# Kernel optimization log

Measured on AMD Instinct MI355X. Metric: run time of the kernel, lower is better.

The kernel has to match this reference:

```python
import jax, jax.numpy as jnp
import numpy as np

B, C, H, W = 32, 1536, 24, 24
HID, D, K = 512, 128, 64  # hidden, cluster_dim, num_clusters


def setup_inputs() -> dict:
    key = jax.random.key(0)
    ks = jax.random.split(key, 6)
    def rn(k, shape, scale):
        return jax.random.normal(k, shape, dtype=jnp.float32) * scale
    return {
        "x": rn(ks[0], (B, C, H, W), 1.0),
        # cluster_features: Conv2d(C,512,1) -> ReLU -> Conv2d(512,D,1)
        "w1c": rn(ks[1], (HID, C), 0.02), "b1c": jnp.zeros((HID,), jnp.float32),
        "w2c": rn(ks[2], (D, HID), 0.02), "b2c": jnp.zeros((D,), jnp.float32),
        # score: Conv2d(C,512,1) -> ReLU -> Conv2d(512,K,1)
        "w1s": rn(ks[3], (HID, C), 0.02), "b1s": jnp.zeros((HID,), jnp.float32),
        "w2s": rn(ks[4], (K, HID), 0.02), "b2s": jnp.zeros((K,), jnp.float32),
        "temperature": jnp.array(1.0, jnp.float32),
    }


def _sinkhorn_log(S, num_iters=3):
    # log-domain OT solver with uniform marginals log(1/n), reg=1 (M/reg == M)
    b, m, n = S.shape
    norm = -jnp.log(jnp.asarray(n, S.dtype))
    log_a = jnp.full((b, m), norm, S.dtype)
    log_b = jnp.full((b, n), norm, S.dtype)
    u = jnp.zeros((b, m), S.dtype)
    v = jnp.zeros((b, n), S.dtype)
    for _ in range(num_iters):
        u = log_a - jax.nn.logsumexp(S + v[:, None, :], axis=2)
        v = log_b - jax.nn.logsumexp(S + u[:, :, None], axis=1)
    # get_matching_probs subtracts norm at the end
    return S + u[:, :, None] + v[:, None, :] - norm


def reference(x, w1c, b1c, w2c, b2c, w1s, b1s, w2s, b2s, temperature):
    b, c, h, w = x.shape
    xf = x.reshape(b, c, h * w)  # (B, C, N); 1x1 conv == channel GEMM
    # cluster features f: (B, D, N)
    hc = jax.nn.relu(jnp.einsum('oc,bcn->bon', w1c, xf) + b1c[None, :, None])
    f = jnp.einsum('oc,bcn->bon', w2c, hc) + b2c[None, :, None]
    # assignment scores p: (B, K, N)
    hs = jax.nn.relu(jnp.einsum('oc,bcn->bon', w1s, xf) + b1s[None, :, None])
    s = jnp.einsum('oc,bcn->bon', w2s, hs) + b2s[None, :, None]
    log_p = _sinkhorn_log(s, num_iters=3)
    p = jnp.exp(log_p / temperature) + jnp.exp(log_p)  # (B, K, N)
    # (f.unsqueeze(2) * p.unsqueeze(1)).sum(-1) == batched matmul
    agg = jnp.einsum('bcn,bkn->bck', f, p)  # (B, D, K)
    flat = agg.reshape(b, -1)
    nrm = jnp.maximum(jnp.linalg.norm(flat, axis=-1, keepdims=True), 1e-12)
    return flat / nrm
```

## Files before the change

kernel.cpp:

```cpp
#include <hip/hip_runtime.h>

typedef unsigned short ushort_t;
typedef float f32x4 __attribute__((ext_vector_type(4)));
typedef short short8 __attribute__((ext_vector_type(8)));

#define B_   32
#define C_   1536
#define N_   576
#define HID_ 512
#define D_   128
#define K_   64

__device__ __forceinline__ float bf2f(ushort_t u) {
    union { unsigned u; float f; } c; c.u = ((unsigned)u) << 16; return c.f;
}
__device__ __forceinline__ ushort_t f2bf(float x) {
    unsigned u = __float_as_uint(x);
    return (ushort_t)((u + 0x7FFFu + ((u >> 16) & 1u)) >> 16);
}

typedef const __attribute__((address_space(1))) char gas_char;
typedef __attribute__((address_space(3))) char las_char;
__device__ __forceinline__ void cp16(const void* g, void* l) {
    __builtin_amdgcn_global_load_lds((gas_char*)(size_t)g,
                                     (las_char*)(unsigned)(size_t)l, 16, 0, 0);
}
__device__ __forceinline__ void bar() {
    asm volatile("" ::: "memory");
    __builtin_amdgcn_s_barrier();
    asm volatile("" ::: "memory");
}

#define OB1_  1572864
#define OW2C_ 1573888
#define OB2C_ 1639424
#define OW2S_ 1639552
#define OB2S_ 1672320
#define WTOT_ 1672384
#define TRB2_ 3456
#define CVB4_ (((WTOT_ / 4) + 255) / 256)

__global__ __launch_bounds__(256) void prep_kernel(
    const void* __restrict__ x,
    const void* __restrict__ w1c, const void* __restrict__ b1c,
    const void* __restrict__ w2c, const void* __restrict__ b2c,
    const void* __restrict__ w1s, const void* __restrict__ b1s,
    const void* __restrict__ w2s, const void* __restrict__ b2s,
    const unsigned* __restrict__ temp,
    ushort_t* __restrict__ xt, ushort_t* __restrict__ o, float* __restrict__ Tp)
{
    __shared__ ushort_t t[128][65];
    unsigned d = temp[0];
    int flag = (d == 0x3F800000u) ? 1 : 0;
    int tid = threadIdx.x;
    int idx = blockIdx.x;
    if (idx == 0 && tid == 0)
        *Tp = flag ? __uint_as_float(d) : bf2f((ushort_t)(d & 0xFFFFu));

    if (idx < TRB2_) {
        int b = idx / 108, rem = idx % 108;
        int c0 = (rem % 12) * 128, n0 = (rem / 12) * 64;
        ushort_t* xtb = xt + (size_t)b * N_ * C_;
        int r = tid >> 4, n4 = (tid & 15) * 4;
        if (flag) {
            const float* xb = (const float*)x + (size_t)b * C_ * N_;
#pragma unroll
            for (int i = 0; i < 8; ++i) {
                int cc = r + i * 16;
                float4 v = *(const float4*)&xb[(size_t)(c0 + cc) * N_ + n0 + n4];
                t[cc][n4 + 0] = f2bf(v.x);
                t[cc][n4 + 1] = f2bf(v.y);
                t[cc][n4 + 2] = f2bf(v.z);
                t[cc][n4 + 3] = f2bf(v.w);
            }
        } else {
            const ushort_t* xb = (const ushort_t*)x + (size_t)b * C_ * N_;
#pragma unroll
            for (int i = 0; i < 8; ++i) {
                int cc = r + i * 16;
                *(uint2*)&t[cc][n4] =
                    *(const uint2*)&xb[(size_t)(c0 + cc) * N_ + n0 + n4];
            }
        }
        __syncthreads();
        int c8 = (tid & 15) * 8;
#pragma unroll
        for (int i = 0; i < 4; ++i) {
            int nn = r + i * 16;
            ushort_t vv[8];
#pragma unroll
            for (int j = 0; j < 8; ++j) vv[j] = t[c8 + j][nn];
            uint4 o4;
            o4.x = (unsigned)vv[0] | ((unsigned)vv[1] << 16);
            o4.y = (unsigned)vv[2] | ((unsigned)vv[3] << 16);
            o4.z = (unsigned)vv[4] | ((unsigned)vv[5] << 16);
            o4.w = (unsigned)vv[6] | ((unsigned)vv[7] << 16);
            *(uint4*)&xtb[(size_t)(n0 + nn) * C_ + c0 + c8] = o4;
        }
    } else {
        int i4 = ((idx - TRB2_) * 256 + tid) * 4;
        if (i4 >= WTOT_) return;
        const void* p; int off;
        if      (i4 < 786432)  { p = w1c; off = i4; }
        else if (i4 < OB1_)    { p = w1s; off = i4 - 786432; }
        else if (i4 < 1573376) { p = b1c; off = i4 - OB1_; }
        else if (i4 < OW2C_)   { p = b1s; off = i4 - 1573376; }
        else if (i4 < OB2C_)   { p = w2c; off = i4 - OW2C_; }
        else if (i4 < OW2S_)   { p = b2c; off = i4 - OB2C_; }
        else if (i4 < OB2S_)   { p = w2s; off = i4 - OW2S_; }
        else                   { p = b2s; off = i4 - OB2S_; }
        if (flag) {
            float4 v = *(const float4*)((const float*)p + off);
            uint2 r;
            r.x = (unsigned)f2bf(v.x) | ((unsigned)f2bf(v.y) << 16);
            r.y = (unsigned)f2bf(v.z) | ((unsigned)f2bf(v.w) << 16);
            *(uint2*)&o[i4] = r;
        } else {
            *(uint2*)&o[i4] = *(const uint2*)((const ushort_t*)p + off);
        }
    }
}

__global__ __launch_bounds__(256) void gemm1_kernel(
    const ushort_t* __restrict__ Xt, const ushort_t* __restrict__ W1,
    const ushort_t* __restrict__ bias, ushort_t* __restrict__ h)
{
    __shared__ ushort_t Atile[2][128 * 64];
    __shared__ ushort_t Btile[2][128 * 64];
    int idx = blockIdx.x;
    int l = (idx & 7) * 144 + (idx >> 3);
    int mt = l >> 3, t = l & 7;
    int row0 = mt * 128, col0 = t * 128;

    int tid = threadIdx.x, w = tid >> 6, lane = tid & 63;
    int wr = w >> 1, wc = w & 1;
    int r16 = lane & 15, q = lane >> 4, kh = q * 8;

    int srow = tid >> 3;
    int cx = ((tid & 7) ^ (srow & 7)) * 8;
    const ushort_t* ag[4];
    const ushort_t* bg[4];
#pragma unroll
    for (int s = 0; s < 4; ++s) {
        ag[s] = Xt + (size_t)(row0 + s * 32 + srow) * C_ + cx;
        bg[s] = W1 + (size_t)(col0 + s * 32 + srow) * C_ + cx;
    }

    f32x4 acc[4][4];
#pragma unroll
    for (int i = 0; i < 4; ++i)
#pragma unroll
        for (int j = 0; j < 4; ++j) acc[i][j] = f32x4{0.f, 0.f, 0.f, 0.f};

    int rowa = wr * 64 + r16;
    int rowb = wc * 64 + r16;
    int xr = (r16 & 7) * 8;

    auto stage = [&](int buf, int koff) {
#pragma unroll
        for (int s = 0; s < 4; ++s) {
            cp16(ag[s] + koff, &Atile[buf][tid * 8 + s * 2048]);
            cp16(bg[s] + koff, &Btile[buf][tid * 8 + s * 2048]);
        }
    };
    auto compute = [&](int cb) {
#pragma unroll
        for (int ks = 0; ks < 2; ++ks) {
            int ke = (ks * 32 + kh) ^ xr;
            short8 af[4], bf[4];
#pragma unroll
            for (int i = 0; i < 4; ++i)
                af[i] = *(const short8*)&Atile[cb][(rowa + i * 16) * 64 + ke];
#pragma unroll
            for (int j = 0; j < 4; ++j)
                bf[j] = *(const short8*)&Btile[cb][(rowb + j * 16) * 64 + ke];
#pragma unroll
            for (int i = 0; i < 4; ++i)
#pragma unroll
                for (int j = 0; j < 4; ++j)
                    acc[i][j] = __builtin_amdgcn_mfma_f32_16x16x32_bf16(
                        af[i], bf[j], acc[i][j], 0, 0, 0);
        }
    };

    stage(0, 0);
#pragma unroll
    for (int kt = 0; kt < 24; ++kt) {
        int buf = kt & 1;
        if (kt < 23) {
            stage(buf ^ 1, (kt + 1) * 64);
            asm volatile("s_waitcnt vmcnt(8)" ::: "memory");
        } else {
            asm volatile("s_waitcnt vmcnt(0)" ::: "memory");
        }
        bar();
        compute(buf);
        bar();
    }

#pragma unroll
    for (int j = 0; j < 4; ++j) {
        int col = col0 + wc * 64 + j * 16 + r16;
        float cb = bf2f(bias[col]);
#pragma unroll
        for (int i = 0; i < 4; ++i) {
            int rowo = row0 + wr * 64 + i * 16 + q * 4;
#pragma unroll
            for (int r = 0; r < 4; ++r) {
                float v = fmaxf(acc[i][j][r] + cb, 0.f);
                h[(size_t)(rowo + r) * 1024 + col] = f2bf(v);
            }
        }
    }
}

__global__ __launch_bounds__(256) void gemm2_kernel(
    const ushort_t* __restrict__ Wb, const ushort_t* __restrict__ h,
    ushort_t* __restrict__ fbuf, float* __restrict__ sbuf)
{
    __shared__ ushort_t Atile[2][128 * 32];
    __shared__ ushort_t Btile[2][128 * 32];
    int nt = blockIdx.x, b = blockIdx.y, z = blockIdx.z;
    int col0 = nt * 128;
    int Mclamp = z ? K_ : D_;
    const ushort_t* Aw   = Wb + (z ? OW2S_ : OW2C_);
    const ushort_t* bias = Wb + (z ? OB2S_ : OB2C_);
    const ushort_t* hb = h + (size_t)b * N_ * 1024 + (z ? 512 : 0);

    int tid = threadIdx.x, w = tid >> 6, lane = tid & 63;
    int wr = w >> 1, wc = w & 1;
    int r16 = lane & 15, q = lane >> 4, kh = q * 8;

    int srow = tid >> 2;
    int swz = ((tid & 3) ^ (srow & 3)) * 8;
    int ar0 = min(srow, Mclamp - 1);
    int ar1 = min(64 + srow, Mclamp - 1);
    const ushort_t* ag0 = Aw + (size_t)ar0 * HID_ + swz;
    const ushort_t* ag1 = Aw + (size_t)ar1 * HID_ + swz;
    int br0 = min(col0 + srow, N_ - 1);
    int br1 = min(col0 + 64 + srow, N_ - 1);
    const ushort_t* bg0 = hb + (size_t)br0 * 1024 + swz;
    const ushort_t* bg1 = hb + (size_t)br1 * 1024 + swz;

    f32x4 acc[4][4];
#pragma unroll
    for (int i = 0; i < 4; ++i)
#pragma unroll
        for (int j = 0; j < 4; ++j) acc[i][j] = f32x4{0.f, 0.f, 0.f, 0.f};

    int xr = (r16 & 3) * 8;

    auto stage = [&](int buf, int koff) {
        cp16(ag0 + koff, &Atile[buf][tid * 8]);
        cp16(ag1 + koff, &Atile[buf][2048 + tid * 8]);
        cp16(bg0 + koff, &Btile[buf][tid * 8]);
        cp16(bg1 + koff, &Btile[buf][2048 + tid * 8]);
    };
    auto compute = [&](int cb) {
        int ke = kh ^ xr;
        short8 af[4], bf[4];
#pragma unroll
        for (int i = 0; i < 4; ++i)
            af[i] = *(const short8*)&Atile[cb][(wr * 64 + i * 16 + r16) * 32 + ke];
#pragma unroll
        for (int j = 0; j < 4; ++j)
            bf[j] = *(const short8*)&Btile[cb][(wc * 64 + j * 16 + r16) * 32 + ke];
#pragma unroll
        for (int i = 0; i < 4; ++i)
#pragma unroll
            for (int j = 0; j < 4; ++j)
                acc[i][j] = __builtin_amdgcn_mfma_f32_16x16x32_bf16(
                    af[i], bf[j], acc[i][j], 0, 0, 0);
    };

    stage(0, 0);
#pragma unroll
    for (int kt = 0; kt < 16; ++kt) {
        int buf = kt & 1;
        if (kt < 15) {
            stage(buf ^ 1, (kt + 1) * 32);
            asm volatile("s_waitcnt vmcnt(4)" ::: "memory");
        } else {
            asm volatile("s_waitcnt vmcnt(0)" ::: "memory");
        }
        bar();
        compute(buf);
        bar();
    }

#pragma unroll
    for (int j = 0; j < 4; ++j) {
        int col = col0 + wc * 64 + j * 16 + r16;
#pragma unroll
        for (int i = 0; i < 4; ++i) {
            int rowb = wr * 64 + i * 16 + q * 4;
#pragma unroll
            for (int r = 0; r < 4; ++r) {
                int rr = rowb + r;
                if (rr < Mclamp && col < N_) {
                    float v = acc[i][j][r] + bf2f(bias[rr]);
                    if (z == 0)
                        fbuf[(size_t)b * D_ * N_ + (size_t)rr * N_ + col] = f2bf(v);
                    else
                        sbuf[(size_t)b * K_ * N_ + (size_t)rr * N_ + col] = v;
                }
            }
        }
    }
}

__global__ __launch_bounds__(512) void tail_kernel(
    const ushort_t* __restrict__ f_all, const float* __restrict__ s_all,
    const float* __restrict__ Tp, const unsigned* __restrict__ temp,
    void* __restrict__ out)
{
    __shared__ float Sl[K_ * 577];
    __shared__ float su[K_];
    __shared__ float sv[N_];
    __shared__ float red[8];
    ushort_t* Plds = (ushort_t*)Sl;
    ushort_t* At0  = (ushort_t*)((char*)Sl + 81920);
    ushort_t* At1  = (ushort_t*)((char*)Sl + 81920 + 16384);

    int b = blockIdx.x;
    int tid = threadIdx.x, w = tid >> 6, lane = tid & 63;
    const float norm = -logf((float)N_);

    const float4* S4 = (const float4*)(s_all + (size_t)b * K_ * N_);
    for (int g = tid; g < (K_ * N_) / 4; g += 512) {
        float4 v = S4[g];
        int w0 = g * 4;
        int r = w0 / N_;
        int base = w0 + r;
        Sl[base + 0] = v.x; Sl[base + 1] = v.y;
        Sl[base + 2] = v.z; Sl[base + 3] = v.w;
    }
    for (int n = tid; n < N_; n += 512) sv[n] = 0.f;
    __syncthreads();

    for (int it = 0; it < 3; ++it) {
        for (int r = w; r < K_; r += 8) {
            const float* Sr = Sl + r * 577;
            float a0 = 0.f, a1 = 0.f, a2 = 0.f;
#pragma unroll
            for (int k = 0; k < 9; k += 3) {
                int n0 = lane + 64 * k;
                a0 += __expf(Sr[n0] + sv[n0]);
                a1 += __expf(Sr[n0 + 64] + sv[n0 + 64]);
                a2 += __expf(Sr[n0 + 128] + sv[n0 + 128]);
            }
            float t = a0 + a1 + a2;
#pragma unroll
            for (int off = 32; off; off >>= 1) t += __shfl_xor(t, off);
            if (lane == 0) su[r] = norm - __logf(t);
        }
        __syncthreads();
        for (int n = tid; n < N_; n += 512) {
            const float* Sc = Sl + n;
            float a0 = 0.f, a1 = 0.f, a2 = 0.f, a3 = 0.f;
#pragma unroll
            for (int m = 0; m < K_; m += 4) {
                a0 += __expf(Sc[(m + 0) * 577] + su[m + 0]);
                a1 += __expf(Sc[(m + 1) * 577] + su[m + 1]);
                a2 += __expf(Sc[(m + 2) * 577] + su[m + 2]);
                a3 += __expf(Sc[(m + 3) * 577] + su[m + 3]);
            }
            sv[n] = norm - __logf((a0 + a1) + (a2 + a3));
        }
        __syncthreads();
    }

    float invT = 1.f / (*Tp);
    ushort_t pv[8][9];
#pragma unroll
    for (int rr = 0; rr < 8; ++rr) {
        int r = w * 8 + rr;
        float ur = su[r];
        const float* Sr = Sl + r * 577;
#pragma unroll
        for (int k = 0; k < 9; ++k) {
            int n0 = lane + 64 * k;
            float lp = Sr[n0] + ur + sv[n0] - norm;
            pv[rr][k] = f2bf(__expf(lp * invT) + __expf(lp));
        }
    }
    __syncthreads();
#pragma unroll
    for (int rr = 0; rr < 8; ++rr) {
        int r = w * 8 + rr;
#pragma unroll
        for (int k = 0; k < 9; ++k)
            Plds[r * 584 + lane + 64 * k] = pv[rr][k];
    }
    __syncthreads();

    int wr = w >> 2, wc = w & 3;
    int r16 = lane & 15, q = lane >> 4, kh = q * 8;
    const ushort_t* F = f_all + (size_t)b * D_ * N_;
    int srow = tid >> 3;
    int cx = ((tid & 7) ^ (srow & 7)) * 8;
    const ushort_t* fg0 = F + (size_t)srow * N_ + cx;
    const ushort_t* fg1 = F + (size_t)(64 + srow) * N_ + cx;

    f32x4 acc[4];
#pragma unroll
    for (int i = 0; i < 4; ++i) acc[i] = f32x4{0.f, 0.f, 0.f, 0.f};

    int rowa = wr * 64 + r16;
    int prow = wc * 16 + r16;
    int xr = (r16 & 7) * 8;

    auto stageF = [&](ushort_t* At, int koff) {
        cp16(fg0 + koff, At + tid * 8);
        cp16(fg1 + koff, At + 4096 + tid * 8);
    };
    auto computeT = [&](const ushort_t* At, int s) {
#pragma unroll
        for (int ks = 0; ks < 2; ++ks) {
            int ke = (ks * 32 + kh) ^ xr;
            short8 af[4];
#pragma unroll
            for (int i = 0; i < 4; ++i)
                af[i] = *(const short8*)&At[(rowa + i * 16) * 64 + ke];
            short8 pf = *(const short8*)&Plds[prow * 584 + s * 64 + ks * 32 + kh];
#pragma unroll
            for (int i = 0; i < 4; ++i)
                acc[i] = __builtin_amdgcn_mfma_f32_16x16x32_bf16(
                    af[i], pf, acc[i], 0, 0, 0);
        }
    };

    stageF(At0, 0);
#pragma unroll
    for (int kt = 0; kt < 9; ++kt) {
        ushort_t* cb = (kt & 1) ? At1 : At0;
        ushort_t* nb = (kt & 1) ? At0 : At1;
        if (kt < 8) {
            stageF(nb, (kt + 1) * 64);
            asm volatile("s_waitcnt vmcnt(2)" ::: "memory");
        } else {
            asm volatile("s_waitcnt vmcnt(0)" ::: "memory");
        }
        bar();
        computeT(cb, kt);
        bar();
    }

    float ssq = 0.f;
#pragma unroll
    for (int i = 0; i < 4; ++i)
#pragma unroll
        for (int r = 0; r < 4; ++r) { float v = acc[i][r]; ssq += v * v; }
#pragma unroll
    for (int off = 32; off; off >>= 1) ssq += __shfl_xor(ssq, off);
    if (lane == 0) red[w] = ssq;
    __syncthreads();
    float tot = (red[0] + red[1] + red[2] + red[3])
              + (red[4] + red[5] + red[6] + red[7]);
    float inv = 1.f / fmaxf(sqrtf(tot), 1e-12f);
    int flag = (temp[0] == 0x3F800000u) ? 1 : 0;
#pragma unroll
    for (int i = 0; i < 4; ++i) {
        int col = wc * 16 + r16;
#pragma unroll
        for (int r = 0; r < 4; ++r) {
            int row = wr * 64 + i * 16 + q * 4 + r;
            float v = acc[i][r] * inv;
            size_t idx = (size_t)b * D_ * K_ + (size_t)row * K_ + col;
            if (flag) ((float*)out)[idx] = v;
            else      ((ushort_t*)out)[idx] = f2bf(v);
        }
    }
}

extern "C" void kernel_launch(void* const* d_in, const int* in_sizes, int n_in,
                              void* d_out, int out_size, void* d_ws, size_t ws_size,
                              hipStream_t stream) {
    const void* x    = d_in[0];
    const void* w1c  = d_in[1];
    const void* b1c  = d_in[2];
    const void* w2c  = d_in[3];
    const void* b2c  = d_in[4];
    const void* w1s  = d_in[5];
    const void* b1s  = d_in[6];
    const void* w2s  = d_in[7];
    const void* b2s  = d_in[8];
    const unsigned* temp = (const unsigned*)d_in[9];

    char* ws = (char*)d_ws;
    float* Tp = (float*)ws;
    ushort_t* Wb = (ushort_t*)(ws + 256);
    size_t offXt = 256 + (((size_t)WTOT_ * 2 + 255) & ~(size_t)255);
    ushort_t* Xt = (ushort_t*)(ws + offXt);
    size_t xtBytes = (size_t)B_ * N_ * C_ * 2;
    ushort_t* h  = (ushort_t*)(ws + offXt + xtBytes);
    size_t o0 = offXt;
    ushort_t* fbuf = (ushort_t*)(ws + o0);  o0 += (size_t)B_ * D_ * N_ * 2;
    float*    sbuf = (float*)(ws + o0);     o0 += (size_t)B_ * K_ * N_ * 4;

    prep_kernel<<<dim3(TRB2_ + CVB4_), 256, 0, stream>>>(
        x, w1c, b1c, w2c, b2c, w1s, b1s, w2s, b2s, temp, Xt, Wb, Tp);
    gemm1_kernel<<<dim3(1152), 256, 0, stream>>>(Xt, Wb, Wb + OB1_, h);
    gemm2_kernel<<<dim3(5, B_, 2), 256, 0, stream>>>(Wb, h, fbuf, sbuf);
    tail_kernel<<<dim3(B_), 512, 0, stream>>>(fbuf, sbuf, Tp, temp, (void*)d_out);
}
```

Baseline: 302.9 us.

## Rewrite gemm1 as single-wave 128x128 tile with B fragments loaded to registers

The first GEMM kernel goes from four waves per 128x128 tile to a single 64-thread wave that owns the whole tile with 8x8 MFMA accumulators. Only A goes through LDS, with a 32-wide K step and swizzle. B fragments are loaded straight from global memory into registers and double-buffered, and the block-wide barriers are replaced by per-wave waitcnt sequencing. This removes barrier overhead and halves LDS traffic, but needs a very large register footprint (256 accumulator floats) and leaves far fewer waves per CU to hide latency.

```diff
diff --git a/kernel.cpp b/kernel.cpp
--- a/kernel.cpp
+++ b/kernel.cpp
@@ -121,90 +121,93 @@
     }
 }
 
-__global__ __launch_bounds__(256) void gemm1_kernel(
+__global__ __launch_bounds__(64, 1) void gemm1_kernel(
     const ushort_t* __restrict__ Xt, const ushort_t* __restrict__ W1,
     const ushort_t* __restrict__ bias, ushort_t* __restrict__ h)
 {
-    __shared__ ushort_t Atile[2][128 * 64];
-    __shared__ ushort_t Btile[2][128 * 64];
+    __shared__ ushort_t Atile[2][128 * 32];
     int idx = blockIdx.x;
     int l = (idx & 7) * 144 + (idx >> 3);
     int mt = l >> 3, t = l & 7;
     int row0 = mt * 128, col0 = t * 128;
 
-    int tid = threadIdx.x, w = tid >> 6, lane = tid & 63;
-    int wr = w >> 1, wc = w & 1;
+    int lane = threadIdx.x;
     int r16 = lane & 15, q = lane >> 4, kh = q * 8;
 
-    int srow = tid >> 3;
-    int cx = ((tid & 7) ^ (srow & 7)) * 8;
-    const ushort_t* ag[4];
-    const ushort_t* bg[4];
-#pragma unroll
-    for (int s = 0; s < 4; ++s) {
-        ag[s] = Xt + (size_t)(row0 + s * 32 + srow) * C_ + cx;
-        bg[s] = W1 + (size_t)(col0 + s * 32 + srow) * C_ + cx;
-    }
-
-    f32x4 acc[4][4];
-#pragma unroll
-    for (int i = 0; i < 4; ++i)
-#pragma unroll
-        for (int j = 0; j < 4; ++j) acc[i][j] = f32x4{0.f, 0.f, 0.f, 0.f};
-
-    int rowa = wr * 64 + r16;
-    int rowb = wc * 64 + r16;
-    int xr = (r16 & 7) * 8;
-
-    auto stage = [&](int buf, int koff) {
-#pragma unroll
-        for (int s = 0; s < 4; ++s) {
-            cp16(ag[s] + koff, &Atile[buf][tid * 8 + s * 2048]);
-            cp16(bg[s] + koff, &Btile[buf][tid * 8 + s * 2048]);
-        }
-    };
-    auto compute = [&](int cb) {
-#pragma unroll
-        for (int ks = 0; ks < 2; ++ks) {
-            int ke = (ks * 32 + kh) ^ xr;
-            short8 af[4], bf[4];
-#pragma unroll
-            for (int i = 0; i < 4; ++i)
-                af[i] = *(const short8*)&Atile[cb][(rowa + i * 16) * 64 + ke];
-#pragma unroll
-            for (int j = 0; j < 4; ++j)
-                bf[j] = *(const short8*)&Btile[cb][(rowb + j * 16) * 64 + ke];
-#pragma unroll
-            for (int i = 0; i < 4; ++i)
-#pragma unroll
-                for (int j = 0; j < 4; ++j)
-                    acc[i][j] = __builtin_amdgcn_mfma_f32_16x16x32_bf16(
-                        af[i], bf[j], acc[i][j], 0, 0, 0);
-        }
-    };
-
-    stage(0, 0);
-#pragma unroll
-    for (int kt = 0; kt < 24; ++kt) {
-        int buf = kt & 1;
-        if (kt < 23) {
-            stage(buf ^ 1, (kt + 1) * 64);
-            asm volatile("s_waitcnt vmcnt(8)" ::: "memory");
-        } else {
-            asm volatile("s_waitcnt vmcnt(0)" ::: "memory");
-        }
-        bar();
-        compute(buf);
-        bar();
-    }
-
-#pragma unroll
-    for (int j = 0; j < 4; ++j) {
-        int col = col0 + wc * 64 + j * 16 + r16;
+    int arow = lane >> 2;
+    int achk = (lane & 3) ^ (arow & 3);
+    const ushort_t* ag[8];
+#pragma unroll
+    for (int c = 0; c < 8; ++c)
+        ag[c] = Xt + (size_t)(row0 + c * 16 + arow) * C_ + achk * 8;
+
+    const ushort_t* bg[8];
+#pragma unroll
+    for (int j = 0; j < 8; ++j)
+        bg[j] = W1 + (size_t)(col0 + j * 16 + r16) * C_ + kh;
+
+    f32x4 acc[8][8];
+#pragma unroll
+    for (int i = 0; i < 8; ++i)
+#pragma unroll
+        for (int j = 0; j < 8; ++j) acc[i][j] = f32x4{0.f, 0.f, 0.f, 0.f};
+
+    int xrc = (q ^ (r16 & 3)) * 8;
+    short8 af[8], bfA[8], bfB[8];
+
+    auto stageA = [&](int buf) {
+#pragma unroll
+        for (int c = 0; c < 8; ++c) {
+            cp16(ag[c], &Atile[buf][c * 512 + lane * 8]);
+            ag[c] += 32;
+        }
+    };
+    auto loadB = [&](short8* bf) {
+#pragma unroll
+        for (int j = 0; j < 8; ++j) {
+            bf[j] = *(const short8*)bg[j];
+            bg[j] += 32;
+        }
+    };
+    auto readA = [&](int buf) {
+#pragma unroll
+        for (int i = 0; i < 8; ++i)
+            af[i] = *(const short8*)&Atile[buf][(i * 16 + r16) * 32 + xrc];
+    };
+    auto domfma = [&](short8* bf) {
+#pragma unroll
+        for (int i = 0; i < 8; ++i)
+#pragma unroll
+            for (int j = 0; j < 8; ++j)
+                acc[i][j] = __builtin_amdgcn_mfma_f32_16x16x32_bf16(
+                    af[i], bf[j], acc[i][j], 0, 0, 0);
+    };
+
+    stageA(0); loadB(bfA); stageA(1); loadB(bfB);
+
+    for (int it = 0; it < 24; ++it) {
+        asm volatile("s_waitcnt vmcnt(16)" ::: "memory");
+        readA(0);
+        asm volatile("s_waitcnt lgkmcnt(0)" ::: "memory");
+        if (it < 23) stageA(0);
+        domfma(bfA);
+        if (it < 23) loadB(bfA);
+        if (it < 23) asm volatile("s_waitcnt vmcnt(16)" ::: "memory");
+        else         asm volatile("s_waitcnt vmcnt(0)"  ::: "memory");
+        readA(1);
+        asm volatile("s_waitcnt lgkmcnt(0)" ::: "memory");
+        if (it < 23) stageA(1);
+        domfma(bfB);
+        if (it < 23) loadB(bfB);
+    }
+
+#pragma unroll
+    for (int j = 0; j < 8; ++j) {
+        int col = col0 + j * 16 + r16;
         float cb = bf2f(bias[col]);
 #pragma unroll
-        for (int i = 0; i < 4; ++i) {
-            int rowo = row0 + wr * 64 + i * 16 + q * 4;
+        for (int i = 0; i < 8; ++i) {
+            int rowo = row0 + i * 16 + q * 4;
 #pragma unroll
             for (int r = 0; r < 4; ++r) {
                 float v = fmaxf(acc[i][j][r] + cb, 0.f);
@@ -500,7 +503,7 @@
 
     prep_kernel<<<dim3(TRB2_ + CVB4_), 256, 0, stream>>>(
         x, w1c, b1c, w2c, b2c, w1s, b1s, w2s, b2s, temp, Xt, Wb, Tp);
-    gemm1_kernel<<<dim3(1152), 256, 0, stream>>>(Xt, Wb, Wb + OB1_, h);
+    gemm1_kernel<<<dim3(1152), 64, 0, stream>>>(Xt, Wb, Wb + OB1_, h);
     gemm2_kernel<<<dim3(5, B_, 2), 256, 0, stream>>>(Wb, h, fbuf, sbuf);
     tail_kernel<<<dim3(B_), 512, 0, stream>>>(fbuf, sbuf, Tp, temp, (void*)d_out);
 }
```

New measurement: 359.4 us. 1.19x slower.

## Load GEMM1 weight fragments directly from global into registers, bypassing LDS

Applied to the files above, without the earlier changes.

The first GEMM kernel no longer stages the W1 (B operand) tile through shared memory. Each wave now loads its own MFMA B fragments straight from global memory into a double-buffered register array, with the wait count adjusted for the extra loads. This halves LDS usage and removes the B-side LDS reads, which could improve occupancy and cut LDS traffic. In exchange, waves that share columns load the same B data twice, the global accesses are only 64-byte contiguous per row, and about 64 more VGPRs are live.

```diff
diff --git a/kernel.cpp b/kernel.cpp
--- a/kernel.cpp
+++ b/kernel.cpp
@@ -126,7 +126,6 @@
     const ushort_t* __restrict__ bias, ushort_t* __restrict__ h)
 {
     __shared__ ushort_t Atile[2][128 * 64];
-    __shared__ ushort_t Btile[2][128 * 64];
     int idx = blockIdx.x;
     int l = (idx & 7) * 144 + (idx >> 3);
     int mt = l >> 3, t = l & 7;
@@ -139,12 +138,14 @@
     int srow = tid >> 3;
     int cx = ((tid & 7) ^ (srow & 7)) * 8;
     const ushort_t* ag[4];
-    const ushort_t* bg[4];
-#pragma unroll
-    for (int s = 0; s < 4; ++s) {
+#pragma unroll
+    for (int s = 0; s < 4; ++s)
         ag[s] = Xt + (size_t)(row0 + s * 32 + srow) * C_ + cx;
-        bg[s] = W1 + (size_t)(col0 + s * 32 + srow) * C_ + cx;
-    }
+
+    const ushort_t* bgp[4];
+#pragma unroll
+    for (int j = 0; j < 4; ++j)
+        bgp[j] = W1 + (size_t)(col0 + wc * 64 + j * 16 + r16) * C_ + kh;
 
     f32x4 acc[4][4];
 #pragma unroll
@@ -152,44 +153,49 @@
 #pragma unroll
         for (int j = 0; j < 4; ++j) acc[i][j] = f32x4{0.f, 0.f, 0.f, 0.f};
 
+    short8 bfr[2][2][4];
+
     int rowa = wr * 64 + r16;
-    int rowb = wc * 64 + r16;
     int xr = (r16 & 7) * 8;
 
-    auto stage = [&](int buf, int koff) {
-#pragma unroll
-        for (int s = 0; s < 4; ++s) {
+    auto stageA = [&](int buf, int koff) {
+#pragma unroll
+        for (int s = 0; s < 4; ++s)
             cp16(ag[s] + koff, &Atile[buf][tid * 8 + s * 2048]);
-            cp16(bg[s] + koff, &Btile[buf][tid * 8 + s * 2048]);
-        }
+    };
+    auto loadB = [&](int buf, int koff) {
+#pragma unroll
+        for (int ks = 0; ks < 2; ++ks)
+#pragma unroll
+            for (int j = 0; j < 4; ++j)
+                bfr[buf][ks][j] = *(const short8*)(bgp[j] + koff + ks * 32);
     };
     auto compute = [&](int cb) {
 #pragma unroll
         for (int ks = 0; ks < 2; ++ks) {
             int ke = (ks * 32 + kh) ^ xr;
-            short8 af[4], bf[4];
+            short8 af[4];
 #pragma unroll
             for (int i = 0; i < 4; ++i)
                 af[i] = *(const short8*)&Atile[cb][(rowa + i * 16) * 64 + ke];
 #pragma unroll
-            for (int j = 0; j < 4; ++j)
-                bf[j] = *(const short8*)&Btile[cb][(rowb + j * 16) * 64 + ke];
-#pragma unroll
             for (int i = 0; i < 4; ++i)
 #pragma unroll
                 for (int j = 0; j < 4; ++j)
                     acc[i][j] = __builtin_amdgcn_mfma_f32_16x16x32_bf16(
-                        af[i], bf[j], acc[i][j], 0, 0, 0);
-        }
-    };
-
-    stage(0, 0);
+                        af[i], bfr[cb][ks][j], acc[i][j], 0, 0, 0);
+        }
+    };
+
+    stageA(0, 0);
+    loadB(0, 0);
 #pragma unroll
     for (int kt = 0; kt < 24; ++kt) {
         int buf = kt & 1;
         if (kt < 23) {
-            stage(buf ^ 1, (kt + 1) * 64);
-            asm volatile("s_waitcnt vmcnt(8)" ::: "memory");
+            stageA(buf ^ 1, (kt + 1) * 64);
+            loadB(buf ^ 1, (kt + 1) * 64);
+            asm volatile("s_waitcnt vmcnt(12)" ::: "memory");
         } else {
             asm volatile("s_waitcnt vmcnt(0)" ::: "memory");
         }
```

New measurement: 371.5 us. +22.6%, slower.
